# Optimization experiments

Measured on AMD Instinct MI355X. Metric: run time of the kernel, lower is better.

Reference implementation:

```python
import jax, jax.numpy as jnp
import numpy as np

ALPHA_MIN = 0.08
ALPHA_MAX = 0.45
BETA = 0.12
SIG_SLOPE = 8.0
SIG_OFFSET = 1.5
EPS = 1e-12


def setup_inputs() -> dict:
    key = jax.random.key(0)
    k1, k2, k3 = jax.random.split(key, 3)
    B, F, T = 8, 64, 2048
    phases = jax.random.normal(k1, (B, F, T), dtype=jnp.float32) * jnp.float32(np.pi)
    prev_coh = jax.random.uniform(k2, (B,), dtype=jnp.float32)  # coherence in [0,1)
    # previous alpha lives in [alpha_min, alpha_max]
    prev_alpha = ALPHA_MIN + (ALPHA_MAX - ALPHA_MIN) * jax.random.uniform(k3, (B,), dtype=jnp.float32)
    return {"phases": phases, "prev_coh": prev_coh, "prev_alpha": prev_alpha}


def reference(phases, prev_coh, prev_alpha):
    phases = phases.astype(jnp.float32)
    # phase-locking value per channel: |mean_t exp(i*phase)|  -> [B, F]
    plv = jnp.abs(jnp.mean(jnp.exp(1j * phases), axis=-1))
    # pairwise phase differences: diff[b,f,g,t] = phases[b,f,t] - phases[b,g,t]
    diff = phases[..., :, None, :] - phases[..., None, :, :]          # [B, F, F, T]
    triad = diff + jnp.swapaxes(diff, -2, -3)                          # [B, F, F, T] (identically 0)
    triad_mag = jnp.abs(jnp.mean(jnp.exp(1j * triad), axis=-1))        # [B, F, F]
    diag = jnp.diagonal(triad_mag, axis1=-2, axis2=-1)                 # [B, F]
    coh = jnp.clip(jnp.mean(jnp.sqrt(plv * diag + EPS), axis=-1), 0.0, 1.0)  # [B]
    # sigmoid hysteresis EMA update (non-empty-state branch)
    velocity = coh - prev_coh
    target_alpha = ALPHA_MIN + (ALPHA_MAX - ALPHA_MIN) * jax.nn.sigmoid(
        SIG_SLOPE * jnp.abs(velocity) - SIG_OFFSET)
    alpha = prev_alpha + BETA * (target_alpha - prev_alpha)            # lerp(prev, target, beta)
    smoothed = alpha * coh + (1.0 - alpha) * prev_coh
    return smoothed
```

## Files before the change

kernel.cpp:

```cpp
#include <hip/hip_runtime.h>
#include <math.h>

#define FCH 64
#define TLEN 2048

__global__ __launch_bounds__(256) void plv_kernel(
    const float* __restrict__ phases, float* __restrict__ ws) {
    const int bf  = blockIdx.x;
    const int tid = threadIdx.x;
    const float4* p = (const float4*)(phases + (size_t)bf * TLEN);

    float cs = 0.0f, ss = 0.0f;
#pragma unroll
    for (int i = 0; i < 2; ++i) {
        float4 v = p[i * 256 + tid];
        float s, c;
        sincosf(v.x, &s, &c); cs += c; ss += s;
        sincosf(v.y, &s, &c); cs += c; ss += s;
        sincosf(v.z, &s, &c); cs += c; ss += s;
        sincosf(v.w, &s, &c); cs += c; ss += s;
    }

#pragma unroll
    for (int off = 32; off > 0; off >>= 1) {
        cs += __shfl_down(cs, off);
        ss += __shfl_down(ss, off);
    }
    __shared__ float scs[4], sss[4];
    const int wave = tid >> 6;
    if ((tid & 63) == 0) { scs[wave] = cs; sss[wave] = ss; }
    __syncthreads();
    if (tid == 0) {
        float c = scs[0] + scs[1] + scs[2] + scs[3];
        float s = sss[0] + sss[1] + sss[2] + sss[3];
        float plv = sqrtf(c * c + s * s) * (1.0f / (float)TLEN);
        ws[bf] = sqrtf(plv + 1e-12f);
    }
}

__global__ __launch_bounds__(512) void finish_kernel(
    const float* __restrict__ ws,
    const float* __restrict__ prev_coh,
    const float* __restrict__ prev_alpha,
    float* __restrict__ out, int B) {
    const int tid = threadIdx.x;
    const int b = tid >> 6;
    float s = (b < B) ? ws[tid] : 0.0f;
#pragma unroll
    for (int off = 32; off > 0; off >>= 1) s += __shfl_down(s, off);
    if ((tid & 63) == 0 && b < B) {
        float coh = s * (1.0f / (float)FCH);
        coh = fminf(fmaxf(coh, 0.0f), 1.0f);
        float pc = prev_coh[b];
        float v = coh - pc;
        float x = 8.0f * fabsf(v) - 1.5f;
        float sig = 1.0f / (1.0f + expf(-x));
        float target = 0.08f + (0.45f - 0.08f) * sig;
        float pa = prev_alpha[b];
        float alpha = pa + 0.12f * (target - pa);
        out[b] = alpha * coh + (1.0f - alpha) * pc;
    }
}

extern "C" void kernel_launch(void* const* d_in, const int* in_sizes, int n_in,
                              void* d_out, int out_size, void* d_ws, size_t ws_size,
                              hipStream_t stream) {
    const float* phases     = (const float*)d_in[0];
    const float* prev_coh   = (const float*)d_in[1];
    const float* prev_alpha = (const float*)d_in[2];
    float* out = (float*)d_out;
    float* ws  = (float*)d_ws;

    const int B = in_sizes[1];
    const int n_bf = B * FCH;

    plv_kernel<<<n_bf, 256, 0, stream>>>(phases, ws);
    finish_kernel<<<1, n_bf, 0, stream>>>(ws, prev_coh, prev_alpha, out, B);
}
```

Before: 59.73 us.

## Fuse PLV and finish kernels into one per-batch block with fast sincos

Replaces the two-kernel pipeline (one block per channel, then a single-block finisher) with one kernel that launches a 1024-thread block per batch item. Each wave reduces four channels, the results go through shared memory, and wave 0 applies the EMA update. It also swaps sincosf for the fast __sinf/__cosf intrinsics. This removes a launch and the workspace round trip, but only 8 blocks run on a GPU with many CUs, so parallelism drops sharply. The fast intrinsics may lose accuracy for phases of a few times pi.

```diff
diff --git a/kernel.cpp b/kernel.cpp
--- a/kernel.cpp
+++ b/kernel.cpp
@@ -4,61 +4,60 @@
 #define FCH 64
 #define TLEN 2048
 
-__global__ __launch_bounds__(256) void plv_kernel(
-    const float* __restrict__ phases, float* __restrict__ ws) {
-    const int bf  = blockIdx.x;
-    const int tid = threadIdx.x;
-    const float4* p = (const float4*)(phases + (size_t)bf * TLEN);
+__global__ __launch_bounds__(1024) void fused_kernel(
+    const float* __restrict__ phases,
+    const float* __restrict__ prev_coh,
+    const float* __restrict__ prev_alpha,
+    float* __restrict__ out) {
+    const int b    = blockIdx.x;
+    const int tid  = threadIdx.x;
+    const int wave = tid >> 6;
+    const int lane = tid & 63;
 
-    float cs = 0.0f, ss = 0.0f;
-#pragma unroll
-    for (int i = 0; i < 2; ++i) {
-        float4 v = p[i * 256 + tid];
-        float s, c;
-        sincosf(v.x, &s, &c); cs += c; ss += s;
-        sincosf(v.y, &s, &c); cs += c; ss += s;
-        sincosf(v.z, &s, &c); cs += c; ss += s;
-        sincosf(v.w, &s, &c); cs += c; ss += s;
-    }
+    __shared__ float chn[FCH];
 
 #pragma unroll
-    for (int off = 32; off > 0; off >>= 1) {
-        cs += __shfl_down(cs, off);
-        ss += __shfl_down(ss, off);
+    for (int k = 0; k < 4; ++k) {
+        const int ch = wave * 4 + k;
+        const float4* p =
+            (const float4*)(phases + ((size_t)b * FCH + ch) * TLEN);
+        float cs = 0.0f, ss = 0.0f;
+#pragma unroll
+        for (int i = 0; i < 8; ++i) {
+            float4 v = p[i * 64 + lane];
+            cs += __cosf(v.x); ss += __sinf(v.x);
+            cs += __cosf(v.y); ss += __sinf(v.y);
+            cs += __cosf(v.z); ss += __sinf(v.z);
+            cs += __cosf(v.w); ss += __sinf(v.w);
+        }
+#pragma unroll
+        for (int off = 32; off > 0; off >>= 1) {
+            cs += __shfl_down(cs, off);
+            ss += __shfl_down(ss, off);
+        }
+        if (lane == 0) {
+            float plv = sqrtf(cs * cs + ss * ss) * (1.0f / (float)TLEN);
+            chn[ch] = sqrtf(plv + 1e-12f);
+        }
     }
-    __shared__ float scs[4], sss[4];
-    const int wave = tid >> 6;
-    if ((tid & 63) == 0) { scs[wave] = cs; sss[wave] = ss; }
     __syncthreads();
-    if (tid == 0) {
-        float c = scs[0] + scs[1] + scs[2] + scs[3];
-        float s = sss[0] + sss[1] + sss[2] + sss[3];
-        float plv = sqrtf(c * c + s * s) * (1.0f / (float)TLEN);
-        ws[bf] = sqrtf(plv + 1e-12f);
-    }
-}
 
-__global__ __launch_bounds__(512) void finish_kernel(
-    const float* __restrict__ ws,
-    const float* __restrict__ prev_coh,
-    const float* __restrict__ prev_alpha,
-    float* __restrict__ out, int B) {
-    const int tid = threadIdx.x;
-    const int b = tid >> 6;
-    float s = (b < B) ? ws[tid] : 0.0f;
+    if (wave == 0) {
+        float s = chn[lane];
 #pragma unroll
-    for (int off = 32; off > 0; off >>= 1) s += __shfl_down(s, off);
-    if ((tid & 63) == 0 && b < B) {
-        float coh = s * (1.0f / (float)FCH);
-        coh = fminf(fmaxf(coh, 0.0f), 1.0f);
-        float pc = prev_coh[b];
-        float v = coh - pc;
-        float x = 8.0f * fabsf(v) - 1.5f;
-        float sig = 1.0f / (1.0f + expf(-x));
-        float target = 0.08f + (0.45f - 0.08f) * sig;
-        float pa = prev_alpha[b];
-        float alpha = pa + 0.12f * (target - pa);
-        out[b] = alpha * coh + (1.0f - alpha) * pc;
+        for (int off = 32; off > 0; off >>= 1) s += __shfl_down(s, off);
+        if (lane == 0) {
+            float coh = s * (1.0f / (float)FCH);
+            coh = fminf(fmaxf(coh, 0.0f), 1.0f);
+            float pc  = prev_coh[b];
+            float vel = coh - pc;
+            float x   = 8.0f * fabsf(vel) - 1.5f;
+            float sig = 1.0f / (1.0f + expf(-x));
+            float target = 0.08f + (0.45f - 0.08f) * sig;
+            float pa  = prev_alpha[b];
+            float alpha = pa + 0.12f * (target - pa);
+            out[b] = alpha * coh + (1.0f - alpha) * pc;
+        }
     }
 }
 
@@ -69,11 +68,7 @@
     const float* prev_coh   = (const float*)d_in[1];
     const float* prev_alpha = (const float*)d_in[2];
     float* out = (float*)d_out;
-    float* ws  = (float*)d_ws;
+    const int B = in_sizes[1];
 
-    const int B = in_sizes[1];
-    const int n_bf = B * FCH;
-
-    plv_kernel<<<n_bf, 256, 0, stream>>>(phases, ws);
-    finish_kernel<<<1, n_bf, 0, stream>>>(ws, prev_coh, prev_alpha, out, B);
+    fused_kernel<<<B, 1024, 0, stream>>>(phases, prev_coh, prev_alpha, out);
 }
```

Measured after the change: 66.06 us. 1.11x slower.
